# Kernel tuning notes

Hardware: AMD Instinct MI355X
Metric: run time of the kernel (lower is better)

## Reference

```python
import jax, jax.numpy as jnp
import numpy as np

N = 20000      # nodes (single node type)
E = 320000     # edges per relation (avg degree 16)
R = 3          # relations / edge types
L = 3          # layers
H = 4          # heads
D = 64         # dim per head (hid_size // n_heads)
IN = 256       # in_size == hid_size
OUT = 128      # out_size
NEG_SLOPE = 0.2


def setup_inputs() -> dict:
    key = jax.random.key(0)
    ks = jax.random.split(key, 8)
    x = jax.random.normal(ks[0], (N, IN), jnp.float32)
    edge_src = jax.random.randint(ks[1], (R, E), 0, N, dtype=jnp.int32)
    edge_dst = jax.random.randint(ks[2], (R, E), 0, N, dtype=jnp.int32)
    W = jax.random.normal(ks[3], (L, R, IN, H * D), jnp.float32) * (1.0 / np.sqrt(IN))
    attn_l = jax.random.normal(ks[4], (L, R, H, D), jnp.float32) * 0.1
    attn_r = jax.random.normal(ks[5], (L, R, H, D), jnp.float32) * 0.1
    bias = jnp.zeros((L, R, H * D), jnp.float32)
    fc_w = jax.random.normal(ks[6], (IN, OUT), jnp.float32) * (1.0 / np.sqrt(IN))
    fc_b = jnp.zeros((OUT,), jnp.float32)
    return dict(x=x, edge_src=edge_src, edge_dst=edge_dst, W=W,
                attn_l=attn_l, attn_r=attn_r, bias=bias, fc_w=fc_w, fc_b=fc_b)


def _gat_conv(h, src, dst, W_r, al, ar, b_r):
    # h: [N, IN] -> feat: [N, H, D]
    feat = (h @ W_r).reshape(N, H, D)
    el = jnp.sum(feat * al, axis=-1)                      # [N, H]
    er = jnp.sum(feat * ar, axis=-1)                      # [N, H]
    e = jax.nn.leaky_relu(el[src] + er[dst], NEG_SLOPE)   # [E, H]
    # segment softmax over incoming edges of each dst node, per head
    m = jax.ops.segment_max(e, dst, num_segments=N)       # [N, H]
    a = jnp.exp(e - m[dst])
    s = jax.ops.segment_sum(a, dst, num_segments=N)       # [N, H]
    alpha = a / s[dst]                                    # [E, H]
    # weighted scatter-add of source features: [N, H, D]
    out = jax.ops.segment_sum(alpha[:, :, None] * feat[src], dst, num_segments=N)
    return out + b_r.reshape(1, H, D)


def reference(x, edge_src, edge_dst, W, attn_l, attn_r, bias, fc_w, fc_b):
    h = x
    for l in range(L):
        acc = jnp.zeros((N, H, D), h.dtype)
        for r in range(R):  # sum-aggregate across relations (HeteroGraphConv aggregate='sum')
            acc = acc + _gat_conv(h, edge_src[r], edge_dst[r],
                                  W[l, r], attn_l[l, r], attn_r[l, r], bias[l, r])
        h = acc.reshape(N, H * D)
        if l != L - 1:
            h = jax.nn.relu(h)  # dropout = identity in eval
    return h @ fc_w + fc_b  # [N, OUT]
```

## Files before the change

### kernel.cpp

```cpp
#include <hip/hip_runtime.h>
#include <math.h>

#define NN 20000
#define NN_PAD 20096
#define EE 320000
#define RR 3
#define LL 3
#define HH 4
#define DD 64
#define CDIM 256
#define OUTD 128
#define NEG 0.2f

#define CVT_N4 (NN * CDIM / 4)
#define CVT_BLK ((CVT_N4 + 255) / 256)
#define CNT_BLK ((RR * EE + 255) / 256)
#define PREP_BLK (8 * 8 * (LL * RR + 1))

typedef float f32x4 __attribute__((ext_vector_type(4)));
typedef short sh8 __attribute__((ext_vector_type(8)));

__device__ __forceinline__ ushort f2bf(float f) {
    union { float f; uint u; } v; v.f = f;
    uint r = (v.u + 0x7FFF + ((v.u >> 16) & 1)) >> 16;
    return (ushort)r;
}
__device__ __forceinline__ float bf2f(ushort u) {
    union { uint u; float f; } v; v.u = ((uint)u) << 16;
    return v.f;
}
__device__ __forceinline__ float bflo(uint p) { return bf2f((ushort)(p & 0xffff)); }
__device__ __forceinline__ float bfhi(uint p) { return bf2f((ushort)(p >> 16)); }

__device__ __forceinline__ void glds16(const ushort* g, ushort* l) {
    __builtin_amdgcn_global_load_lds(
        (const __attribute__((address_space(1))) void*)g,
        (__attribute__((address_space(3))) void*)l, 16, 0, 0);
}

__global__ __launch_bounds__(256) void fused_cvt_count(
    const float* __restrict__ in, ushort* __restrict__ out,
    const int* __restrict__ edge_dst, int* __restrict__ deg) {
    int bid = blockIdx.x;
    if (bid < CVT_BLK) {
        int i = bid * 256 + threadIdx.x;
        if (i >= CVT_N4) return;
        float4 v = *(const float4*)(in + (size_t)i * 4);
        ushort4 o;
        o.x = f2bf(v.x); o.y = f2bf(v.y); o.z = f2bf(v.z); o.w = f2bf(v.w);
        *(ushort4*)(out + (size_t)i * 4) = o;
    } else {
        int i = (bid - CVT_BLK) * 256 + threadIdx.x;
        if (i >= RR * EE) return;
        int r = i / EE;
        atomicAdd(&deg[r * NN + edge_dst[i]], 1);
    }
}

__global__ __launch_bounds__(1024) void scan_kernel(
    const int* __restrict__ deg, int* __restrict__ row_ptr, int* __restrict__ cursor) {
    int r = blockIdx.x;
    const int* d = deg + r * NN;
    int* rp = row_ptr + r * (NN + 1);
    int* cur = cursor + r * (NN + 1);
    __shared__ int wsum[16];
    int lane = threadIdx.x & 63, wv = threadIdx.x >> 6;
    if (threadIdx.x == 0) { rp[0] = 0; cur[0] = 0; }
    int carry = 0;
    for (int base = 0; base < NN; base += 1024) {
        int i = base + threadIdx.x;
        int v = (i < NN) ? d[i] : 0;
        int s = v;
        #pragma unroll
        for (int off = 1; off < 64; off <<= 1) {
            int n = __shfl_up(s, off, 64);
            if (lane >= off) s += n;
        }
        if (lane == 63) wsum[wv] = s;
        __syncthreads();
        if (wv == 0) {
            int ws = (lane < 16) ? wsum[lane] : 0;
            #pragma unroll
            for (int off = 1; off < 16; off <<= 1) {
                int n = __shfl_up(ws, off, 64);
                if (lane >= off) ws += n;
            }
            if (lane < 16) wsum[lane] = ws;
        }
        __syncthreads();
        int incl = carry + (wv ? wsum[wv - 1] : 0) + s;
        if (i < NN) { rp[i + 1] = incl; cur[i + 1] = incl; }
        carry += wsum[15];
        __syncthreads();
    }
}

__global__ __launch_bounds__(256) void fused_fill_prep(
    const int* __restrict__ edge_src, const int* __restrict__ edge_dst,
    int* __restrict__ cursor, int* __restrict__ csr_src,
    const float* __restrict__ W, const float* __restrict__ fc_w,
    ushort* __restrict__ Wt, ushort* __restrict__ fct) {
    __shared__ float tile[32][33];
    int bid = blockIdx.x;
    if (bid < CNT_BLK) {
        int i = bid * 256 + threadIdx.x;
        if (i >= RR * EE) return;
        int r = i / EE;
        int dst = edge_dst[i];
        int pos = atomicAdd(&cursor[r * (NN + 1) + dst], 1);
        csr_src[r * EE + pos] = edge_src[i];
        return;
    }
    int q = bid - CNT_BLK;
    int z = q >> 6;
    int rem = q & 63;
    int by = rem >> 3, bx = rem & 7;
    int tx = threadIdx.x & 31, ty = threadIdx.x >> 5;
    const float* src;
    ushort* dst;
    int N;
    if (z < LL * RR) {
        src = W + (size_t)z * CDIM * CDIM;
        dst = Wt + (size_t)z * CDIM * CDIM;
        N = CDIM;
    } else {
        src = fc_w;
        dst = fct;
        N = OUTD;
    }
    int kb = bx * 32, nb = by * 32;
    if (nb >= N) return;
    for (int yy = ty; yy < 32; yy += 8)
        tile[yy][tx] = src[(size_t)(kb + yy) * N + nb + tx];
    __syncthreads();
    for (int yy = ty; yy < 32; yy += 8)
        dst[(size_t)(nb + yy) * CDIM + kb + tx] = f2bf(tile[tx][yy]);
}


#define TM 128
#define TN 128
#define TK 32

__global__ __launch_bounds__(256) void gemm_bf16(
    const ushort* __restrict__ A, const ushort* __restrict__ Bt0, void* __restrict__ C0,
    int M, int K, int Ncol, long strideB, long strideC,
    const float* __restrict__ bias, int out_fp32,
    const float* __restrict__ al_all, const float* __restrict__ ar_all,
    float* __restrict__ el_all, float* __restrict__ er_all) {
    __shared__ alignas(16) ushort As[TM * 32];
    __shared__ alignas(16) ushort Bs[TN * 32];
    const ushort* Bt = Bt0 + (size_t)blockIdx.z * strideB;
    int m0 = blockIdx.x * TM, n0 = blockIdx.y * TN;
    int t = threadIdx.x;
    int wave = t >> 6, lane = t & 63;
    int q = lane >> 4, l16 = lane & 15;
    int wrow = (wave >> 1) * 64, wcol = (wave & 1) * 64;

    int sw = (q ^ ((l16 >> 1) & 3)) * 8;
    int a_off[4], b_off[4];
    #pragma unroll
    for (int i = 0; i < 4; i++) {
        a_off[i] = (wrow + i * 16 + l16) * 32 + sw;
        b_off[i] = (wcol + i * 16 + l16) * 32 + sw;
    }
    int row_a = t >> 2;
    int ch_a  = ((t & 3) ^ ((row_a >> 1) & 3)) * 8;

    f32x4 acc[4][4];
    #pragma unroll
    for (int i = 0; i < 4; i++)
        #pragma unroll
        for (int j = 0; j < 4; j++)
            #pragma unroll
            for (int k = 0; k < 4; k++) acc[i][j][k] = 0.f;

    for (int k0 = 0; k0 < K; k0 += TK) {
        #pragma unroll
        for (int s = 0; s < 2; s++) {
            int qid = t + s * 256;
            int row = row_a + s * 64;
            glds16(A + (size_t)(m0 + row) * K + k0 + ch_a, As + qid * 8);
        }
        #pragma unroll
        for (int s = 0; s < 2; s++) {
            int qid = t + s * 256;
            int row = row_a + s * 64;
            glds16(Bt + (size_t)(n0 + row) * K + k0 + ch_a, Bs + qid * 8);
        }
        __syncthreads();
        sh8 af[4], bfr[4];
        #pragma unroll
        for (int i = 0; i < 4; i++) af[i] = *(const sh8*)(As + a_off[i]);
        #pragma unroll
        for (int j = 0; j < 4; j++) bfr[j] = *(const sh8*)(Bs + b_off[j]);
        #pragma unroll
        for (int i = 0; i < 4; i++)
            #pragma unroll
            for (int j = 0; j < 4; j++)
                acc[i][j] = __builtin_amdgcn_mfma_f32_16x16x32_bf16(af[i], bfr[j], acc[i][j], 0, 0, 0);
        __syncthreads();
    }

    if (out_fp32) {
        float* C = (float*)C0 + (size_t)blockIdx.z * strideC;
        #pragma unroll
        for (int i = 0; i < 4; i++) {
            #pragma unroll
            for (int reg = 0; reg < 4; reg++) {
                int row = m0 + wrow + i * 16 + q * 4 + reg;
                if (row >= M) continue;
                #pragma unroll
                for (int j = 0; j < 4; j++) {
                    int col = n0 + wcol + j * 16 + l16;
                    float v = acc[i][j][reg];
                    if (bias) v += bias[col];
                    C[(size_t)row * Ncol + col] = v;
                }
            }
        }
    } else {
        ushort* C = (ushort*)C0 + (size_t)blockIdx.z * strideC;
        #pragma unroll
        for (int i = 0; i < 4; i++) {
            #pragma unroll
            for (int reg = 0; reg < 4; reg++) {
                int row = m0 + wrow + i * 16 + q * 4 + reg;
                if (row >= M) continue;
                #pragma unroll
                for (int j = 0; j < 4; j++) {
                    int col = n0 + wcol + j * 16 + l16;
                    C[(size_t)row * Ncol + col] = f2bf(acc[i][j][reg]);
                }
            }
        }
    }

    if (el_all) {
        const float* al = al_all + (size_t)blockIdx.z * CDIM;
        const float* ar = ar_all + (size_t)blockIdx.z * CDIM;
        float* elp = el_all + (size_t)blockIdx.z * NN * HH;
        float* erp = er_all + (size_t)blockIdx.z * NN * HH;
        int head = (n0 + wcol) >> 6;
        float alj[4], arj[4];
        #pragma unroll
        for (int j = 0; j < 4; j++) {
            int gcol = n0 + wcol + j * 16 + l16;
            alj[j] = al[gcol];
            arj[j] = ar[gcol];
        }
        #pragma unroll
        for (int i = 0; i < 4; i++) {
            #pragma unroll
            for (int reg = 0; reg < 4; reg++) {
                int row = m0 + wrow + i * 16 + q * 4 + reg;
                float pl = 0.f, pr = 0.f;
                #pragma unroll
                for (int j = 0; j < 4; j++) {
                    pl = fmaf(acc[i][j][reg], alj[j], pl);
                    pr = fmaf(acc[i][j][reg], arj[j], pr);
                }
                #pragma unroll
                for (int m = 1; m < 16; m <<= 1) {
                    pl += __shfl_xor(pl, m, 64);
                    pr += __shfl_xor(pr, m, 64);
                }
                if (l16 == 0 && row < M) {
                    elp[(size_t)row * HH + head] = pl;
                    erp[(size_t)row * HH + head] = pr;
                }
            }
        }
    }
}

__global__ __launch_bounds__(256) void aggregate_fused(
    const ushort* __restrict__ feat16, const float* __restrict__ el,
    const float* __restrict__ er, const int* __restrict__ row_ptr,
    const int* __restrict__ csr_src, const float* __restrict__ bias,
    ushort* __restrict__ hout, int relu) {
    int wv = threadIdx.x >> 6, lane = threadIdx.x & 63;
    int node = blockIdx.x * 4 + wv;
    if (node >= NN) return;
    int c0 = lane * 4;
    int h = lane >> 4;
    float t0 = 0.f, t1 = 0.f, t2 = 0.f, t3 = 0.f;
    #pragma unroll
    for (int r = 0; r < RR; r++) {
        const int* rp = row_ptr + r * (NN + 1);
        int beg = rp[node], end = rp[node + 1];
        const ushort* fr = feat16 + (size_t)r * NN * CDIM;
        const float* elr = el + (size_t)r * NN * HH;
        float ern = er[((size_t)r * NN + node) * HH + h];
        const int* cs = csr_src + (size_t)r * EE;
        float p0 = 0.f, p1 = 0.f, p2 = 0.f, p3 = 0.f, ssum = 0.f;
        int e = beg;
        for (; e + 4 <= end; e += 4) {
            int s0 = cs[e], s1 = cs[e + 1], s2 = cs[e + 2], s3 = cs[e + 3];
            float x0 = elr[s0 * HH + h];
            float x1 = elr[s1 * HH + h];
            float x2 = elr[s2 * HH + h];
            float x3 = elr[s3 * HH + h];
            uint2 f0 = *(const uint2*)(fr + (size_t)s0 * CDIM + c0);
            uint2 f1 = *(const uint2*)(fr + (size_t)s1 * CDIM + c0);
            uint2 f2 = *(const uint2*)(fr + (size_t)s2 * CDIM + c0);
            uint2 f3 = *(const uint2*)(fr + (size_t)s3 * CDIM + c0);
            x0 += ern; x1 += ern; x2 += ern; x3 += ern;
            x0 = x0 > 0.f ? x0 : NEG * x0;
            x1 = x1 > 0.f ? x1 : NEG * x1;
            x2 = x2 > 0.f ? x2 : NEG * x2;
            x3 = x3 > 0.f ? x3 : NEG * x3;
            float a0 = __expf(x0), a1 = __expf(x1), a2 = __expf(x2), a3 = __expf(x3);
            ssum += a0 + a1 + a2 + a3;
            p0 = fmaf(a0, bflo(f0.x), p0); p1 = fmaf(a0, bfhi(f0.x), p1);
            p2 = fmaf(a0, bflo(f0.y), p2); p3 = fmaf(a0, bfhi(f0.y), p3);
            p0 = fmaf(a1, bflo(f1.x), p0); p1 = fmaf(a1, bfhi(f1.x), p1);
            p2 = fmaf(a1, bflo(f1.y), p2); p3 = fmaf(a1, bfhi(f1.y), p3);
            p0 = fmaf(a2, bflo(f2.x), p0); p1 = fmaf(a2, bfhi(f2.x), p1);
            p2 = fmaf(a2, bflo(f2.y), p2); p3 = fmaf(a2, bfhi(f2.y), p3);
            p0 = fmaf(a3, bflo(f3.x), p0); p1 = fmaf(a3, bfhi(f3.x), p1);
            p2 = fmaf(a3, bflo(f3.y), p2); p3 = fmaf(a3, bfhi(f3.y), p3);
        }
        for (; e < end; e++) {
            int s = cs[e];
            float x = elr[s * HH + h] + ern;
            x = x > 0.f ? x : NEG * x;
            float a = __expf(x);
            uint2 f = *(const uint2*)(fr + (size_t)s * CDIM + c0);
            ssum += a;
            p0 = fmaf(a, bflo(f.x), p0); p1 = fmaf(a, bfhi(f.x), p1);
            p2 = fmaf(a, bflo(f.y), p2); p3 = fmaf(a, bfhi(f.y), p3);
        }
        float is = (end > beg) ? 1.f / ssum : 0.f;
        t0 += p0 * is + bias[r * CDIM + c0];
        t1 += p1 * is + bias[r * CDIM + c0 + 1];
        t2 += p2 * is + bias[r * CDIM + c0 + 2];
        t3 += p3 * is + bias[r * CDIM + c0 + 3];
    }
    if (relu) {
        t0 = fmaxf(t0, 0.f); t1 = fmaxf(t1, 0.f);
        t2 = fmaxf(t2, 0.f); t3 = fmaxf(t3, 0.f);
    }
    uint2 o;
    o.x = (uint)f2bf(t0) | ((uint)f2bf(t1) << 16);
    o.y = (uint)f2bf(t2) | ((uint)f2bf(t3) << 16);
    *(uint2*)(hout + (size_t)node * CDIM + c0) = o;
}


extern "C" void kernel_launch(void* const* d_in, const int* in_sizes, int n_in,
                              void* d_out, int out_size, void* d_ws, size_t ws_size,
                              hipStream_t stream) {
    const float* x        = (const float*)d_in[0];
    const int*   edge_src = (const int*)d_in[1];
    const int*   edge_dst = (const int*)d_in[2];
    const float* W        = (const float*)d_in[3];
    const float* attn_l   = (const float*)d_in[4];
    const float* attn_r   = (const float*)d_in[5];
    const float* bias     = (const float*)d_in[6];
    const float* fc_w     = (const float*)d_in[7];
    const float* fc_b     = (const float*)d_in[8];
    float* out = (float*)d_out;

    char* ws = (char*)d_ws;
    size_t off = 0;
    auto alloc = [&](size_t bytes) {
        void* p = ws + off;
        off = (off + bytes + 255) & ~(size_t)255;
        return p;
    };
    ushort* x16    = (ushort*)alloc((size_t)NN_PAD * CDIM * 2);
    ushort* h16    = (ushort*)alloc((size_t)NN_PAD * CDIM * 2);
    ushort* feat16 = (ushort*)alloc((size_t)RR * NN * CDIM * 2);
    ushort* Wt16   = (ushort*)alloc((size_t)LL * RR * CDIM * CDIM * 2);
    ushort* fct16  = (ushort*)alloc((size_t)OUTD * CDIM * 2);
    float* el      = (float*)alloc((size_t)RR * NN * HH * 4);
    float* er      = (float*)alloc((size_t)RR * NN * HH * 4);
    int* row_ptr   = (int*)alloc((size_t)RR * (NN + 1) * 4);
    int* cursor    = (int*)alloc((size_t)RR * (NN + 1) * 4);
    int* csr_src   = (int*)alloc((size_t)RR * EE * 4);
    int* deg       = (int*)alloc((size_t)RR * NN * 4);

    hipMemsetAsync(deg, 0, (size_t)RR * NN * 4, stream);
    fused_cvt_count<<<dim3(CVT_BLK + CNT_BLK), dim3(256), 0, stream>>>(
        x, x16, edge_dst, deg);
    scan_kernel<<<dim3(RR), dim3(1024), 0, stream>>>(deg, row_ptr, cursor);
    fused_fill_prep<<<dim3(CNT_BLK + PREP_BLK), dim3(256), 0, stream>>>(
        edge_src, edge_dst, cursor, csr_src, W, fc_w, Wt16, fct16);

    const ushort* hin = x16;
    for (int l = 0; l < LL; l++) {
        const ushort* Wl = Wt16 + (size_t)l * RR * CDIM * CDIM;
        dim3 g(NN_PAD / TM, CDIM / TN, RR);
        gemm_bf16<<<g, dim3(256), 0, stream>>>(hin, Wl, feat16, NN, CDIM, CDIM,
                                               (long)CDIM * CDIM, (long)NN * CDIM, nullptr, 0,
                                               attn_l + (size_t)l * RR * CDIM,
                                               attn_r + (size_t)l * RR * CDIM, el, er);
        aggregate_fused<<<dim3(NN / 4), dim3(256), 0, stream>>>(
            feat16, el, er, row_ptr, csr_src, bias + (size_t)l * RR * CDIM,
            h16, (l != LL - 1) ? 1 : 0);
        hin = h16;
    }
    dim3 gf(NN_PAD / TM, OUTD / TN, 1);
    gemm_bf16<<<gf, dim3(256), 0, stream>>>(h16, fct16, out, NN, CDIM, OUTD,
                                            0, 0, fc_b, 1, nullptr, nullptr, nullptr, nullptr);
}
```

Baseline: 512.0 us.

## Split wavefront into two half-waves gathering alternate edges with 16-byte loads

The aggregation kernel now has each half of the 64-lane wavefront process alternate edges, with every lane loading 8 bf16 channels as one 16-byte vector instead of 4 channels as 8 bytes. This doubles the number of edges in flight per wave. The scalar remainder loop becomes a single masked 8-edge step, and the two halves' partial sums are combined with cross-lane shuffles before the softmax normalisation. The cost is more registers, shuffle reductions, and redundant gathers of the last edge in the masked tail.

Result: no change. 514.5 us (+0.5%).

```diff
diff --git a/kernel.cpp b/kernel.cpp
--- a/kernel.cpp
+++ b/kernel.cpp
@@ -282,9 +282,14 @@
     int wv = threadIdx.x >> 6, lane = threadIdx.x & 63;
     int node = blockIdx.x * 4 + wv;
     if (node >= NN) return;
-    int c0 = lane * 4;
-    int h = lane >> 4;
-    float t0 = 0.f, t1 = 0.f, t2 = 0.f, t3 = 0.f;
+    int half = lane >> 5;
+    int l32 = lane & 31;
+    int ch0 = l32 * 8;
+    int h = l32 >> 3;
+    float t[8];
+    #pragma unroll
+    for (int c = 0; c < 8; c++) t[c] = 0.f;
+
     #pragma unroll
     for (int r = 0; r < RR; r++) {
         const int* rp = row_ptr + r * (NN + 1);
@@ -293,18 +298,24 @@
         const float* elr = el + (size_t)r * NN * HH;
         float ern = er[((size_t)r * NN + node) * HH + h];
         const int* cs = csr_src + (size_t)r * EE;
-        float p0 = 0.f, p1 = 0.f, p2 = 0.f, p3 = 0.f, ssum = 0.f;
+        float p[8];
+        #pragma unroll
+        for (int c = 0; c < 8; c++) p[c] = 0.f;
+        float ssum = 0.f;
         int e = beg;
-        for (; e + 4 <= end; e += 4) {
-            int s0 = cs[e], s1 = cs[e + 1], s2 = cs[e + 2], s3 = cs[e + 3];
-            float x0 = elr[s0 * HH + h];
-            float x1 = elr[s1 * HH + h];
-            float x2 = elr[s2 * HH + h];
-            float x3 = elr[s3 * HH + h];
-            uint2 f0 = *(const uint2*)(fr + (size_t)s0 * CDIM + c0);
-            uint2 f1 = *(const uint2*)(fr + (size_t)s1 * CDIM + c0);
-            uint2 f2 = *(const uint2*)(fr + (size_t)s2 * CDIM + c0);
-            uint2 f3 = *(const uint2*)(fr + (size_t)s3 * CDIM + c0);
+        for (; e + 8 <= end; e += 8) {
+            uint s0 = (uint)cs[e + half];
+            uint s1 = (uint)cs[e + 2 + half];
+            uint s2 = (uint)cs[e + 4 + half];
+            uint s3 = (uint)cs[e + 6 + half];
+            float x0 = elr[(s0 << 2) + h];
+            float x1 = elr[(s1 << 2) + h];
+            float x2 = elr[(s2 << 2) + h];
+            float x3 = elr[(s3 << 2) + h];
+            uint4 f0 = *(const uint4*)(fr + (s0 << 8) + ch0);
+            uint4 f1 = *(const uint4*)(fr + (s1 << 8) + ch0);
+            uint4 f2 = *(const uint4*)(fr + (s2 << 8) + ch0);
+            uint4 f3 = *(const uint4*)(fr + (s3 << 8) + ch0);
             x0 += ern; x1 += ern; x2 += ern; x3 += ern;
             x0 = x0 > 0.f ? x0 : NEG * x0;
             x1 = x1 > 0.f ? x1 : NEG * x1;
@@ -312,39 +323,91 @@
             x3 = x3 > 0.f ? x3 : NEG * x3;
             float a0 = __expf(x0), a1 = __expf(x1), a2 = __expf(x2), a3 = __expf(x3);
             ssum += a0 + a1 + a2 + a3;
-            p0 = fmaf(a0, bflo(f0.x), p0); p1 = fmaf(a0, bfhi(f0.x), p1);
-            p2 = fmaf(a0, bflo(f0.y), p2); p3 = fmaf(a0, bfhi(f0.y), p3);
-            p0 = fmaf(a1, bflo(f1.x), p0); p1 = fmaf(a1, bfhi(f1.x), p1);
-            p2 = fmaf(a1, bflo(f1.y), p2); p3 = fmaf(a1, bfhi(f1.y), p3);
-            p0 = fmaf(a2, bflo(f2.x), p0); p1 = fmaf(a2, bfhi(f2.x), p1);
-            p2 = fmaf(a2, bflo(f2.y), p2); p3 = fmaf(a2, bfhi(f2.y), p3);
-            p0 = fmaf(a3, bflo(f3.x), p0); p1 = fmaf(a3, bfhi(f3.x), p1);
-            p2 = fmaf(a3, bflo(f3.y), p2); p3 = fmaf(a3, bfhi(f3.y), p3);
-        }
-        for (; e < end; e++) {
-            int s = cs[e];
-            float x = elr[s * HH + h] + ern;
-            x = x > 0.f ? x : NEG * x;
-            float a = __expf(x);
-            uint2 f = *(const uint2*)(fr + (size_t)s * CDIM + c0);
-            ssum += a;
-            p0 = fmaf(a, bflo(f.x), p0); p1 = fmaf(a, bfhi(f.x), p1);
-            p2 = fmaf(a, bflo(f.y), p2); p3 = fmaf(a, bfhi(f.y), p3);
-        }
+            p[0] = fmaf(a0, bflo(f0.x), p[0]); p[1] = fmaf(a0, bfhi(f0.x), p[1]);
+            p[2] = fmaf(a0, bflo(f0.y), p[2]); p[3] = fmaf(a0, bfhi(f0.y), p[3]);
+            p[4] = fmaf(a0, bflo(f0.z), p[4]); p[5] = fmaf(a0, bfhi(f0.z), p[5]);
+            p[6] = fmaf(a0, bflo(f0.w), p[6]); p[7] = fmaf(a0, bfhi(f0.w), p[7]);
+            p[0] = fmaf(a1, bflo(f1.x), p[0]); p[1] = fmaf(a1, bfhi(f1.x), p[1]);
+            p[2] = fmaf(a1, bflo(f1.y), p[2]); p[3] = fmaf(a1, bfhi(f1.y), p[3]);
+            p[4] = fmaf(a1, bflo(f1.z), p[4]); p[5] = fmaf(a1, bfhi(f1.z), p[5]);
+            p[6] = fmaf(a1, bflo(f1.w), p[6]); p[7] = fmaf(a1, bfhi(f1.w), p[7]);
+            p[0] = fmaf(a2, bflo(f2.x), p[0]); p[1] = fmaf(a2, bfhi(f2.x), p[1]);
+            p[2] = fmaf(a2, bflo(f2.y), p[2]); p[3] = fmaf(a2, bfhi(f2.y), p[3]);
+            p[4] = fmaf(a2, bflo(f2.z), p[4]); p[5] = fmaf(a2, bfhi(f2.z), p[5]);
+            p[6] = fmaf(a2, bflo(f2.w), p[6]); p[7] = fmaf(a2, bfhi(f2.w), p[7]);
+            p[0] = fmaf(a3, bflo(f3.x), p[0]); p[1] = fmaf(a3, bfhi(f3.x), p[1]);
+            p[2] = fmaf(a3, bflo(f3.y), p[2]); p[3] = fmaf(a3, bfhi(f3.y), p[3]);
+            p[4] = fmaf(a3, bflo(f3.z), p[4]); p[5] = fmaf(a3, bfhi(f3.z), p[5]);
+            p[6] = fmaf(a3, bflo(f3.w), p[6]); p[7] = fmaf(a3, bfhi(f3.w), p[7]);
+        }
+        if (e < end) {
+            int last = end - 1;
+            int j0 = e + half, j1 = e + 2 + half, j2 = e + 4 + half, j3 = e + 6 + half;
+            bool m0 = j0 < end, m1 = j1 < end, m2 = j2 < end, m3 = j3 < end;
+            uint s0 = (uint)cs[m0 ? j0 : last];
+            uint s1 = (uint)cs[m1 ? j1 : last];
+            uint s2 = (uint)cs[m2 ? j2 : last];
+            uint s3 = (uint)cs[m3 ? j3 : last];
+            float x0 = elr[(s0 << 2) + h];
+            float x1 = elr[(s1 << 2) + h];
+            float x2 = elr[(s2 << 2) + h];
+            float x3 = elr[(s3 << 2) + h];
+            uint4 f0 = *(const uint4*)(fr + (s0 << 8) + ch0);
+            uint4 f1 = *(const uint4*)(fr + (s1 << 8) + ch0);
+            uint4 f2 = *(const uint4*)(fr + (s2 << 8) + ch0);
+            uint4 f3 = *(const uint4*)(fr + (s3 << 8) + ch0);
+            x0 += ern; x1 += ern; x2 += ern; x3 += ern;
+            x0 = x0 > 0.f ? x0 : NEG * x0;
+            x1 = x1 > 0.f ? x1 : NEG * x1;
+            x2 = x2 > 0.f ? x2 : NEG * x2;
+            x3 = x3 > 0.f ? x3 : NEG * x3;
+            float a0 = m0 ? __expf(x0) : 0.f;
+            float a1 = m1 ? __expf(x1) : 0.f;
+            float a2 = m2 ? __expf(x2) : 0.f;
+            float a3 = m3 ? __expf(x3) : 0.f;
+            ssum += a0 + a1 + a2 + a3;
+            p[0] = fmaf(a0, bflo(f0.x), p[0]); p[1] = fmaf(a0, bfhi(f0.x), p[1]);
+            p[2] = fmaf(a0, bflo(f0.y), p[2]); p[3] = fmaf(a0, bfhi(f0.y), p[3]);
+            p[4] = fmaf(a0, bflo(f0.z), p[4]); p[5] = fmaf(a0, bfhi(f0.z), p[5]);
+            p[6] = fmaf(a0, bflo(f0.w), p[6]); p[7] = fmaf(a0, bfhi(f0.w), p[7]);
+            p[0] = fmaf(a1, bflo(f1.x), p[0]); p[1] = fmaf(a1, bfhi(f1.x), p[1]);
+            p[2] = fmaf(a1, bflo(f1.y), p[2]); p[3] = fmaf(a1, bfhi(f1.y), p[3]);
+            p[4] = fmaf(a1, bflo(f1.z), p[4]); p[5] = fmaf(a1, bfhi(f1.z), p[5]);
+            p[6] = fmaf(a1, bflo(f1.w), p[6]); p[7] = fmaf(a1, bfhi(f1.w), p[7]);
+            p[0] = fmaf(a2, bflo(f2.x), p[0]); p[1] = fmaf(a2, bfhi(f2.x), p[1]);
+            p[2] = fmaf(a2, bflo(f2.y), p[2]); p[3] = fmaf(a2, bfhi(f2.y), p[3]);
+            p[4] = fmaf(a2, bflo(f2.z), p[4]); p[5] = fmaf(a2, bfhi(f2.z), p[5]);
+            p[6] = fmaf(a2, bflo(f2.w), p[6]); p[7] = fmaf(a2, bfhi(f2.w), p[7]);
+            p[0] = fmaf(a3, bflo(f3.x), p[0]); p[1] = fmaf(a3, bfhi(f3.x), p[1]);
+            p[2] = fmaf(a3, bflo(f3.y), p[2]); p[3] = fmaf(a3, bfhi(f3.y), p[3]);
+            p[4] = fmaf(a3, bflo(f3.z), p[4]); p[5] = fmaf(a3, bfhi(f3.z), p[5]);
+            p[6] = fmaf(a3, bflo(f3.w), p[6]); p[7] = fmaf(a3, bfhi(f3.w), p[7]);
+        }
+        ssum += __shfl_xor(ssum, 32, 64);
         float is = (end > beg) ? 1.f / ssum : 0.f;
-        t0 += p0 * is + bias[r * CDIM + c0];
-        t1 += p1 * is + bias[r * CDIM + c0 + 1];
-        t2 += p2 * is + bias[r * CDIM + c0 + 2];
-        t3 += p3 * is + bias[r * CDIM + c0 + 3];
+        #pragma unroll
+        for (int c = 0; c < 8; c++) {
+            float pc = p[c] + __shfl_xor(p[c], 32, 64);
+            t[c] = fmaf(pc, is, t[c]);
+        }
+        #pragma unroll
+        for (int c = 0; c < 8; c += 2) {
+            float2 b = *(const float2*)(bias + r * CDIM + ch0 + c);
+            t[c] += b.x; t[c + 1] += b.y;
+        }
     }
     if (relu) {
-        t0 = fmaxf(t0, 0.f); t1 = fmaxf(t1, 0.f);
-        t2 = fmaxf(t2, 0.f); t3 = fmaxf(t3, 0.f);
-    }
-    uint2 o;
-    o.x = (uint)f2bf(t0) | ((uint)f2bf(t1) << 16);
-    o.y = (uint)f2bf(t2) | ((uint)f2bf(t3) << 16);
-    *(uint2*)(hout + (size_t)node * CDIM + c0) = o;
+        #pragma unroll
+        for (int c = 0; c < 8; c++) t[c] = fmaxf(t[c], 0.f);
+    }
+    if (half == 0) {
+        uint4 o;
+        o.x = (uint)f2bf(t[0]) | ((uint)f2bf(t[1]) << 16);
+        o.y = (uint)f2bf(t[2]) | ((uint)f2bf(t[3]) << 16);
+        o.z = (uint)f2bf(t[4]) | ((uint)f2bf(t[5]) << 16);
+        o.w = (uint)f2bf(t[6]) | ((uint)f2bf(t[7]) << 16);
+        *(uint4*)(hout + (size_t)node * CDIM + ch0) = o;
+    }
 }
 
 
```
